# Kernel optimization log

Measured on AMD Instinct MI355X. Metric: run time of the kernel, lower is better.

## Reference

```python
import jax, jax.numpy as jnp
import numpy as np

K_NEIGHBOURS = 16
ITERATIONS = 3
NUM_CLASSES = 20
N_POINTS = 20000


def setup_inputs() -> dict:
    key = jax.random.key(0)
    k1, k2 = jax.random.split(key)
    logits = jax.random.normal(k1, (N_POINTS, NUM_CLASSES), dtype=jnp.float32)
    coords = jax.random.uniform(k2, (N_POINTS, 3), dtype=jnp.float32)
    # nn.init.eye_ then *= -0.1
    compat_w = (-0.1 * jnp.eye(NUM_CLASSES, dtype=jnp.float32))
    return {"logits": logits, "coords": coords, "compat_w": compat_w}


def _knn_graph(coords, k):
    # torch.cdist (p=2): euclidean distances, (N, N)
    sq = jnp.sum(coords * coords, axis=-1)
    d2 = sq[:, None] + sq[None, :] - 2.0 * (coords @ coords.T)
    dists = jnp.sqrt(jnp.clip(d2, 0.0))
    # smallest-k -> top_k of negated distances
    _, idx = jax.lax.top_k(-dists, k)  # (N, k)
    return idx


def reference(logits, coords, compat_w):
    knn_idx = _knn_graph(coords, K_NEIGHBOURS)
    q = jax.nn.softmax(logits, axis=-1)
    for _ in range(ITERATIONS):
        neighbour_q = q[knn_idx]            # (N, k, K) gather
        msg = jnp.mean(neighbour_q, axis=1)  # (N, K)
        refined = logits + msg @ compat_w.T  # nn.Linear: x @ W^T
        q = jax.nn.softmax(refined, axis=-1)
    return (refined, q)
```

## Files before the change

kernel.cpp:

```cpp
#include <hip/hip_runtime.h>

#define N_PTS 20000
#define NCLS 20
#define KNN 16
#define GRID 12
#define NCELLS (GRID * GRID * GRID)
#define HCELL (1.0f / (float)GRID)
#define CAND_CAP 640
#define KEY_CAP 128
#define R_TARGET 0.0680f

__device__ __forceinline__ int cell1d(float v) {
    int c = (int)(v * (float)GRID);
    return min(max(c, 0), GRID - 1);
}

__global__ __launch_bounds__(256) void count_scan_kernel(const float* __restrict__ coords,
                                                         int* __restrict__ cellCount,
                                                         int* __restrict__ doneCtr,
                                                         int* __restrict__ cellStart,
                                                         int* __restrict__ cellCursor) {
    const int p = blockIdx.x * blockDim.x + threadIdx.x;
    if (p < N_PTS) {
        const int cx = cell1d(coords[3 * p + 0]);
        const int cy = cell1d(coords[3 * p + 1]);
        const int cz = cell1d(coords[3 * p + 2]);
        atomicAdd(&cellCount[(cz * GRID + cy) * GRID + cx], 1);
    }
    __threadfence();
    __syncthreads();
    __shared__ bool isLast;
    if (threadIdx.x == 0)
        isLast = (atomicAdd(doneCtr, 1) == (int)gridDim.x - 1);
    __syncthreads();
    if (!isLast) return;

    __shared__ int part[256];
    const int t = threadIdx.x;
    const int base = t * 7;
    int local[7];
    int s = 0;
#pragma unroll
    for (int i = 0; i < 7; ++i) {
        const int c = base + i;
        const int v = (c < NCELLS)
            ? __hip_atomic_load(&cellCount[c], __ATOMIC_RELAXED, __HIP_MEMORY_SCOPE_AGENT)
            : 0;
        local[i] = s;
        s += v;
    }
    part[t] = s;
    __syncthreads();
    for (int off = 1; off < 256; off <<= 1) {
        const int v = part[t] + ((t >= off) ? part[t - off] : 0);
        __syncthreads();
        part[t] = v;
        __syncthreads();
    }
    const int excl = (t > 0) ? part[t - 1] : 0;
#pragma unroll
    for (int i = 0; i < 7; ++i) {
        const int c = base + i;
        if (c < NCELLS) {
            cellStart[c] = excl + local[i];
            cellCursor[c] = excl + local[i];
        }
    }
    if (t == 255) cellStart[NCELLS] = part[255];
}

__global__ __launch_bounds__(256) void scatter_kernel(const float* __restrict__ coords,
                                                      const float* __restrict__ logits,
                                                      int* __restrict__ cellCursor,
                                                      float4* __restrict__ sortedPts,
                                                      int* __restrict__ orig,
                                                      float* __restrict__ ls,
                                                      float* __restrict__ q0s) {
    const int p = blockIdx.x * blockDim.x + threadIdx.x;
    if (p >= N_PTS) return;
    const float x = coords[3 * p + 0];
    const float y = coords[3 * p + 1];
    const float z = coords[3 * p + 2];
    const int c = (cell1d(z) * GRID + cell1d(y)) * GRID + cell1d(x);
    const int pos = atomicAdd(&cellCursor[c], 1);
    sortedPts[pos] = make_float4(x, y, z, __uint_as_float((unsigned)p));
    orig[pos] = p;
    const float4* l4 = (const float4*)(logits + p * NCLS);
    float v[NCLS];
#pragma unroll
    for (int u = 0; u < 5; ++u) {
        const float4 a = l4[u];
        v[4 * u + 0] = a.x; v[4 * u + 1] = a.y;
        v[4 * u + 2] = a.z; v[4 * u + 3] = a.w;
    }
    float4* d4 = (float4*)(ls + pos * NCLS);
#pragma unroll
    for (int u = 0; u < 5; ++u)
        d4[u] = make_float4(v[4 * u], v[4 * u + 1], v[4 * u + 2], v[4 * u + 3]);
    float mx = v[0];
#pragma unroll
    for (int cc = 1; cc < NCLS; ++cc) mx = fmaxf(mx, v[cc]);
    float sum = 0.f;
#pragma unroll
    for (int cc = 0; cc < NCLS; ++cc) { v[cc] = __expf(v[cc] - mx); sum += v[cc]; }
    const float inv = 1.f / sum;
    float4* q4 = (float4*)(q0s + pos * NCLS);
#pragma unroll
    for (int u = 0; u < 5; ++u)
        q4[u] = make_float4(v[4 * u] * inv, v[4 * u + 1] * inv,
                            v[4 * u + 2] * inv, v[4 * u + 3] * inv);
}

__device__ void knn_ladder(const float4* __restrict__ sortedPts,
                           const int* __restrict__ cellStart,
                           const float4 qp, const int s, int hw,
                           unsigned long long* keys, const int lane,
                           int* __restrict__ knn_out) {
    const unsigned long long laneLt = (1ull << lane) - 1ull;
    const int cx = cell1d(qp.x), cy = cell1d(qp.y), cz = cell1d(qp.z);
    float g = 0.9995f * (float)hw * HCELL;
    float tau = g * g;
    int cnt = 0;
    for (int att = 0; att < 16; ++att) {
        cnt = 0;
        const int xlo = max(cx - hw, 0), xhi = min(cx + hw, GRID - 1);
        const int ylo = max(cy - hw, 0), yhi = min(cy + hw, GRID - 1);
        const int zlo = max(cz - hw, 0), zhi = min(cz + hw, GRID - 1);
        for (int zz = zlo; zz <= zhi; ++zz) {
            for (int yy = ylo; yy <= yhi; ++yy) {
                const int rowc = (zz * GRID + yy) * GRID;
                const int beg = cellStart[rowc + xlo];
                const int end = cellStart[rowc + xhi + 1];
                for (int j0 = beg; j0 < end; j0 += 64) {
                    const int j = j0 + lane;
                    const bool jv = j < end;
                    const float4 pt = sortedPts[jv ? j : beg];
                    const float dx = pt.x - qp.x, dy = pt.y - qp.y, dz = pt.z - qp.z;
                    const float d2 = dx * dx + dy * dy + dz * dz;
                    const bool take = jv && (d2 < tau);
                    const unsigned long long mm = __ballot(take);
                    if (take) {
                        const int pos = cnt + (int)__popcll(mm & laneLt);
                        if (pos < KEY_CAP)
                            keys[pos] = (((unsigned long long)__float_as_uint(d2)) << 32) |
                                        (unsigned long long)(unsigned)j;
                    }
                    cnt += (int)__popcll(mm);
                }
            }
        }
        if (cnt >= KNN && cnt <= KEY_CAP) break;
        if (cnt < KNN) {
            if (hw < GRID - 1) { ++hw; g = 0.9995f * (float)hw * HCELL; tau = g * g; }
            else tau *= 2.5f;
        } else {
            tau *= 0.6f;
        }
    }
    const int m = min(cnt, KEY_CAP);
    const unsigned long long k0 = (lane < m) ? keys[lane] : ~0ull;
    const unsigned long long k1 = (lane + 64 < m) ? keys[lane + 64] : ~0ull;
    int r0 = 0, r1 = 0;
    for (int j = 0; j < m; ++j) {
        const unsigned long long kj = keys[j];
        r0 += (kj < k0); r1 += (kj < k1);
    }
    if (lane < m && r0 < KNN)      knn_out[s * KNN + r0] = (int)(unsigned)(k0 & 0xffffffffull);
    if (lane + 64 < m && r1 < KNN) knn_out[s * KNN + r1] = (int)(unsigned)(k1 & 0xffffffffull);
}

__global__ __launch_bounds__(256) void knn_kernel(const float4* __restrict__ sortedPts,
                                                  const int* __restrict__ cellStart,
                                                  int* __restrict__ knn_out) {
    __shared__ float4 cand[CAND_CAP];
    __shared__ unsigned long long keys[4][KEY_CAP];
    const int lane = threadIdx.x & 63;
    const int wave = threadIdx.x >> 6;
    const int c = blockIdx.x >> 1;
    const int half = blockIdx.x & 1;
    const int cz = c / (GRID * GRID);
    const int cy = (c / GRID) % GRID;
    const int cx = c % GRID;
    const int pbeg = cellStart[c];
    const int pend = cellStart[c + 1];
    const int npts = pend - pbeg;
    if (npts <= 0) return;
    const int bd = (cx == 0 || cx == GRID - 1) + (cy == 0 || cy == GRID - 1) +
                   (cz == 0 || cz == GRID - 1);
    const int hs = (bd >= 2) ? 2 : 1;
    const unsigned long long laneLt = (1ull << lane) - 1ull;

    const int xlo = max(cx - hs, 0), xhi = min(cx + hs, GRID - 1);
    const int ylo = max(cy - hs, 0), yhi = min(cy + hs, GRID - 1);
    const int zlo = max(cz - hs, 0), zhi = min(cz + hs, GRID - 1);
    const int ny = yhi - ylo + 1;
    const int nruns = (zhi - zlo + 1) * ny;

    int beg = 0, len = 0;
    if (lane < nruns) {
        const int zz = zlo + lane / ny;
        const int yy = ylo + lane % ny;
        const int rowc = (zz * GRID + yy) * GRID;
        beg = cellStart[rowc + xlo];
        len = cellStart[rowc + xhi + 1] - beg;
    }
    int off = len;
#pragma unroll
    for (int sh = 1; sh < 32; sh <<= 1) {
        const int o = __shfl_up(off, sh, 64);
        if (lane >= sh) off += o;
    }
    const int nc = __shfl(off, nruns - 1);
    off -= len;
    const int ownRun = (cz - zlo) * ny + (cy - ylo);
    const int ownOff = __shfl(off, ownRun) + (pbeg - __shfl(beg, ownRun));

    if (nc <= CAND_CAP) {
        for (int r = wave; r < nruns; r += 4) {
            const int rb = __shfl(beg, r);
            const int rl = __shfl(len, r);
            const int ro = __shfl(off, r);
            for (int i = lane; i < rl; i += 64) {
                float4 pt = sortedPts[rb + i];
                pt.w = __uint_as_float((unsigned)(rb + i));
                cand[ro + i] = pt;
            }
        }
    }
    __syncthreads();

    if (nc > CAND_CAP) {
        for (int idx = 2 * wave + half; idx < npts; idx += 8)
            knn_ladder(sortedPts, cellStart, sortedPts[pbeg + idx], pbeg + idx,
                       hs, keys[wave], lane, knn_out);
        return;
    }

    const float taumaxr = 0.9995f * (float)hs * HCELL;
    const float taumax = taumaxr * taumaxr;

    for (int idx = 2 * wave + half; idx < npts; idx += 8) {
        const int s = pbeg + idx;
        const float4 qp = cand[ownOff + idx];
        float r = R_TARGET;
        const float inv2r = 0.5f / r;
        const float fx = (fminf(qp.x + r, 1.f) - fmaxf(qp.x - r, 0.f)) * inv2r;
        const float fy = (fminf(qp.y + r, 1.f) - fmaxf(qp.y - r, 0.f)) * inv2r;
        const float fz = (fminf(qp.z + r, 1.f) - fmaxf(qp.z - r, 0.f)) * inv2r;
        const float f = fmaxf(fx * fy * fz, 0.05f);
        r = R_TARGET * __powf(f, -0.33333334f);
        float tau = fminf(r * r, taumax);
        bool triedMax = (tau >= taumax * 0.999f);

        int cnt = 0;
        bool ok = false;
        for (int att = 0; att < 5 && !ok; ++att) {
            cnt = 0;
            for (int j0 = 0; j0 < nc; j0 += 64) {
                const int j = j0 + lane;
                float d2 = 1e30f;
                unsigned pw = 0;
                if (j < nc) {
                    const float4 pt = cand[j];
                    const float dx = pt.x - qp.x, dy = pt.y - qp.y, dz = pt.z - qp.z;
                    d2 = dx * dx + dy * dy + dz * dz;
                    pw = __float_as_uint(pt.w);
                }
                const bool take = d2 < tau;
                const unsigned long long mm = __ballot(take);
                if (take) {
                    const int pos = cnt + (int)__popcll(mm & laneLt);
                    if (pos < KEY_CAP)
                        keys[wave][pos] =
                            (((unsigned long long)__float_as_uint(d2)) << 32) |
                            (unsigned long long)pw;
                }
                cnt += (int)__popcll(mm);
            }
            if (cnt >= KNN && cnt <= KEY_CAP) ok = true;
            else if (cnt < KNN) {
                if (triedMax) break;
                tau = taumax; triedMax = true;
            } else tau *= 0.6f;
        }
        if (!ok) {
            knn_ladder(sortedPts, cellStart, qp, s, hs + 1, keys[wave], lane, knn_out);
            continue;
        }
        const int m = cnt;
        const unsigned long long k0 = (lane < m) ? keys[wave][lane] : ~0ull;
        const unsigned long long k1 = (lane + 64 < m) ? keys[wave][lane + 64] : ~0ull;
        int r0 = 0, r1 = 0;
        for (int j = 0; j < m; ++j) {
            const unsigned long long kj = keys[wave][j];
            r0 += (kj < k0); r1 += (kj < k1);
        }
        if (lane < m && r0 < KNN)      knn_out[s * KNN + r0] = (int)(unsigned)(k0 & 0xffffffffull);
        if (lane + 64 < m && r1 < KNN) knn_out[s * KNN + r1] = (int)(unsigned)(k1 & 0xffffffffull);
    }
}

__global__ __launch_bounds__(256) void crf_iter_kernel(const float* __restrict__ ls,
                                                       const float* __restrict__ W,
                                                       const int* __restrict__ knn,
                                                       const float* __restrict__ qin,
                                                       float* __restrict__ qout,
                                                       const int* __restrict__ orig,
                                                       float* __restrict__ outRef,
                                                       float* __restrict__ outQ) {
    __shared__ float Ws[NCLS * NCLS];
    for (int i = threadIdx.x; i < NCLS * NCLS; i += blockDim.x) Ws[i] = W[i];
    __syncthreads();
    const int t = blockIdx.x * blockDim.x + threadIdx.x;
    const int p = t >> 2;
    const int qtr = t & 3;
    if (p >= N_PTS) return;

    float acc[NCLS];
#pragma unroll
    for (int c = 0; c < NCLS; ++c) acc[c] = 0.f;

    const int4 k4 = ((const int4*)(knn + p * KNN))[qtr];
    const int ids[4] = {k4.x, k4.y, k4.z, k4.w};
#pragma unroll
    for (int u = 0; u < 4; ++u) {
        unsigned id = (unsigned)ids[u];
        if (id >= N_PTS) id = 0;
        const float4* r4 = (const float4*)(qin + id * NCLS);
#pragma unroll
        for (int v = 0; v < 5; ++v) {
            const float4 a = r4[v];
            acc[4 * v + 0] += a.x; acc[4 * v + 1] += a.y;
            acc[4 * v + 2] += a.z; acc[4 * v + 3] += a.w;
        }
    }
#pragma unroll
    for (int c = 0; c < NCLS; ++c) {
        acc[c] += __shfl_xor(acc[c], 1, 64);
        acc[c] += __shfl_xor(acc[c], 2, 64);
        acc[c] *= (1.f / 16.f);
    }

    const int c0 = qtr * 5;
    float ref[5];
#pragma unroll
    for (int i = 0; i < 5; ++i) {
        float s = ls[p * NCLS + c0 + i];
#pragma unroll
        for (int k = 0; k < NCLS; ++k) s += acc[k] * Ws[(c0 + i) * NCLS + k];
        ref[i] = s;
    }

    float mx = ref[0];
#pragma unroll
    for (int i = 1; i < 5; ++i) mx = fmaxf(mx, ref[i]);
    mx = fmaxf(mx, __shfl_xor(mx, 1, 64));
    mx = fmaxf(mx, __shfl_xor(mx, 2, 64));
    float ex[5];
    float ps = 0.f;
#pragma unroll
    for (int i = 0; i < 5; ++i) { ex[i] = __expf(ref[i] - mx); ps += ex[i]; }
    ps += __shfl_xor(ps, 1, 64);
    ps += __shfl_xor(ps, 2, 64);
    const float inv = 1.f / ps;

    if (outRef != nullptr) {
        const int o = orig[p];
#pragma unroll
        for (int i = 0; i < 5; ++i) {
            outRef[o * NCLS + c0 + i] = ref[i];
            outQ[o * NCLS + c0 + i] = ex[i] * inv;
        }
    } else {
#pragma unroll
        for (int i = 0; i < 5; ++i) qout[p * NCLS + c0 + i] = ex[i] * inv;
    }
}

extern "C" void kernel_launch(void* const* d_in, const int* in_sizes, int n_in,
                              void* d_out, int out_size, void* d_ws, size_t ws_size,
                              hipStream_t stream) {
    const float* logits = (const float*)d_in[0];
    const float* coords = (const float*)d_in[1];
    const float* W      = (const float*)d_in[2];
    float* out = (float*)d_out;

    char* ws = (char*)d_ws;
    size_t off = 0;
    int* knn = (int*)(ws + off);              off += (size_t)N_PTS * KNN * 4;
    off = (off + 255) & ~(size_t)255;
    float* ls = (float*)(ws + off);           off += (size_t)N_PTS * NCLS * 4;
    off = (off + 255) & ~(size_t)255;
    float* q0s = (float*)(ws + off);          off += (size_t)N_PTS * NCLS * 4;
    off = (off + 255) & ~(size_t)255;
    float4* sortedPts = (float4*)(ws + off);  off += (size_t)N_PTS * 16;
    off = (off + 255) & ~(size_t)255;
    int* orig = (int*)(ws + off);             off += (size_t)N_PTS * 4;
    off = (off + 255) & ~(size_t)255;
    int* cellCount = (int*)(ws + off);        off += (size_t)(NCELLS + 1) * 4;
    int* doneCtr = cellCount + NCELLS;
    off = (off + 255) & ~(size_t)255;
    int* cellStart = (int*)(ws + off);        off += (size_t)(NCELLS + 1) * 4;
    off = (off + 255) & ~(size_t)255;
    int* cellCursor = (int*)(ws + off);
    float* q1s = out + N_PTS * NCLS;

    const int threads = 256;
    const int pblocks = (N_PTS + threads - 1) / threads;
    const int cblocks = (4 * N_PTS + threads - 1) / threads;

    hipMemsetAsync(cellCount, 0, (NCELLS + 1) * sizeof(int), stream);
    count_scan_kernel<<<pblocks, threads, 0, stream>>>(coords, cellCount, doneCtr,
                                                       cellStart, cellCursor);
    scatter_kernel<<<pblocks, threads, 0, stream>>>(coords, logits, cellCursor,
                                                    sortedPts, orig, ls, q0s);
    knn_kernel<<<NCELLS * 2, threads, 0, stream>>>(sortedPts, cellStart, knn);
    crf_iter_kernel<<<cblocks, threads, 0, stream>>>(ls, W, knn, q0s, q1s, orig,
                                                     nullptr, nullptr);
    crf_iter_kernel<<<cblocks, threads, 0, stream>>>(ls, W, knn, q1s, q0s, orig,
                                                     nullptr, nullptr);
    crf_iter_kernel<<<cblocks, threads, 0, stream>>>(ls, W, knn, q0s, nullptr, orig,
                                                     out, out + N_PTS * NCLS);
}
```

Before: 128.5 us.

## Fuse count/scan/scatter and CRF iterations into kernels with in-grid barriers

Merges the cell count/scan kernel with the scatter kernel, using a release/acquire flag so the other blocks spin until the last block has finished the prefix scan. Merges the three CRF iteration launches into one kernel with a software grid barrier between iterations, and hoists the knn index and logit loads out of the iteration loop. Also vectorises the rank-counting loop over the shared-memory keys with 16-byte loads. This removes three kernel launches and their gaps, at the risk of deadlock if not all blocks (pblocks=79, cblocks=313) are resident at once, plus the cost of spin-waiting.

```diff
diff --git a/kernel.cpp b/kernel.cpp
--- a/kernel.cpp
+++ b/kernel.cpp
@@ -15,12 +15,15 @@
     return min(max(c, 0), GRID - 1);
 }
 
-__global__ __launch_bounds__(256) void count_scan_kernel(const float* __restrict__ coords,
-                                                         int* __restrict__ cellCount,
-                                                         int* __restrict__ doneCtr,
-                                                         int* __restrict__ cellStart,
-                                                         int* __restrict__ cellCursor) {
+__global__ __launch_bounds__(256) void build_scatter_kernel(
+        const float* __restrict__ coords, const float* __restrict__ logits,
+        int* __restrict__ cellCount, int* __restrict__ doneCtr,
+        int* __restrict__ scanFlag, int* __restrict__ cellStart,
+        int* __restrict__ cellCursor, float4* __restrict__ sortedPts,
+        int* __restrict__ orig, float* __restrict__ ls, float* __restrict__ q0s) {
     const int p = blockIdx.x * blockDim.x + threadIdx.x;
+    const int tid = threadIdx.x;
+
     if (p < N_PTS) {
         const int cx = cell1d(coords[3 * p + 0]);
         const int cy = cell1d(coords[3 * p + 1]);
@@ -30,53 +33,55 @@
     __threadfence();
     __syncthreads();
     __shared__ bool isLast;
-    if (threadIdx.x == 0)
+    if (tid == 0)
         isLast = (atomicAdd(doneCtr, 1) == (int)gridDim.x - 1);
     __syncthreads();
-    if (!isLast) return;
-
-    __shared__ int part[256];
-    const int t = threadIdx.x;
-    const int base = t * 7;
-    int local[7];
-    int s = 0;
-#pragma unroll
-    for (int i = 0; i < 7; ++i) {
-        const int c = base + i;
-        const int v = (c < NCELLS)
-            ? __hip_atomic_load(&cellCount[c], __ATOMIC_RELAXED, __HIP_MEMORY_SCOPE_AGENT)
-            : 0;
-        local[i] = s;
-        s += v;
-    }
-    part[t] = s;
-    __syncthreads();
-    for (int off = 1; off < 256; off <<= 1) {
-        const int v = part[t] + ((t >= off) ? part[t - off] : 0);
+
+    if (isLast) {
+        __shared__ int part[256];
+        const int base = tid * 7;
+        int local[7];
+        int s = 0;
+#pragma unroll
+        for (int i = 0; i < 7; ++i) {
+            const int c = base + i;
+            const int v = (c < NCELLS)
+                ? __hip_atomic_load(&cellCount[c], __ATOMIC_RELAXED, __HIP_MEMORY_SCOPE_AGENT)
+                : 0;
+            local[i] = s;
+            s += v;
+        }
+        part[tid] = s;
         __syncthreads();
-        part[t] = v;
+        for (int off = 1; off < 256; off <<= 1) {
+            const int v = part[tid] + ((tid >= off) ? part[tid - off] : 0);
+            __syncthreads();
+            part[tid] = v;
+            __syncthreads();
+        }
+        const int excl = (tid > 0) ? part[tid - 1] : 0;
+#pragma unroll
+        for (int i = 0; i < 7; ++i) {
+            const int c = base + i;
+            if (c < NCELLS) {
+                cellStart[c] = excl + local[i];
+                __hip_atomic_store(&cellCursor[c], excl + local[i],
+                                   __ATOMIC_RELAXED, __HIP_MEMORY_SCOPE_AGENT);
+            }
+        }
+        if (tid == 255) cellStart[NCELLS] = part[255];
+        __threadfence();
         __syncthreads();
-    }
-    const int excl = (t > 0) ? part[t - 1] : 0;
-#pragma unroll
-    for (int i = 0; i < 7; ++i) {
-        const int c = base + i;
-        if (c < NCELLS) {
-            cellStart[c] = excl + local[i];
-            cellCursor[c] = excl + local[i];
-        }
-    }
-    if (t == 255) cellStart[NCELLS] = part[255];
-}
-
-__global__ __launch_bounds__(256) void scatter_kernel(const float* __restrict__ coords,
-                                                      const float* __restrict__ logits,
-                                                      int* __restrict__ cellCursor,
-                                                      float4* __restrict__ sortedPts,
-                                                      int* __restrict__ orig,
-                                                      float* __restrict__ ls,
-                                                      float* __restrict__ q0s) {
-    const int p = blockIdx.x * blockDim.x + threadIdx.x;
+        if (tid == 0)
+            __hip_atomic_store(scanFlag, 1, __ATOMIC_RELEASE, __HIP_MEMORY_SCOPE_AGENT);
+    } else {
+        if (tid == 0)
+            while (__hip_atomic_load(scanFlag, __ATOMIC_ACQUIRE,
+                                     __HIP_MEMORY_SCOPE_AGENT) == 0) {}
+        __syncthreads();
+        __threadfence();
+    }
+
     if (p >= N_PTS) return;
     const float x = coords[3 * p + 0];
     const float y = coords[3 * p + 1];
@@ -109,6 +114,29 @@
     for (int u = 0; u < 5; ++u)
         q4[u] = make_float4(v[4 * u] * inv, v[4 * u + 1] * inv,
                             v[4 * u + 2] * inv, v[4 * u + 3] * inv);
+}
+
+__device__ __forceinline__ void rank2(const unsigned long long* __restrict__ keys,
+                                      int m, unsigned long long k0,
+                                      unsigned long long k1, int& r0, int& r1) {
+    r0 = 0; r1 = 0;
+    const ulonglong2* kp = (const ulonglong2*)keys;
+    const int mPairs = m >> 1;
+    int j2 = 0;
+    for (; j2 + 4 <= mPairs; j2 += 4) {
+        const ulonglong2 a = kp[j2 + 0];
+        const ulonglong2 b = kp[j2 + 1];
+        const ulonglong2 cc = kp[j2 + 2];
+        const ulonglong2 d = kp[j2 + 3];
+        r0 += (a.x < k0) + (a.y < k0) + (b.x < k0) + (b.y < k0) +
+              (cc.x < k0) + (cc.y < k0) + (d.x < k0) + (d.y < k0);
+        r1 += (a.x < k1) + (a.y < k1) + (b.x < k1) + (b.y < k1) +
+              (cc.x < k1) + (cc.y < k1) + (d.x < k1) + (d.y < k1);
+    }
+    for (int j = j2 * 2; j < m; ++j) {
+        const unsigned long long kj = keys[j];
+        r0 += (kj < k0); r1 += (kj < k1);
+    }
 }
 
 __device__ void knn_ladder(const float4* __restrict__ sortedPts,
@@ -160,11 +188,8 @@
     const int m = min(cnt, KEY_CAP);
     const unsigned long long k0 = (lane < m) ? keys[lane] : ~0ull;
     const unsigned long long k1 = (lane + 64 < m) ? keys[lane + 64] : ~0ull;
-    int r0 = 0, r1 = 0;
-    for (int j = 0; j < m; ++j) {
-        const unsigned long long kj = keys[j];
-        r0 += (kj < k0); r1 += (kj < k1);
-    }
+    int r0, r1;
+    rank2(keys, m, k0, k1, r0, r1);
     if (lane < m && r0 < KNN)      knn_out[s * KNN + r0] = (int)(unsigned)(k0 & 0xffffffffull);
     if (lane + 64 < m && r1 < KNN) knn_out[s * KNN + r1] = (int)(unsigned)(k1 & 0xffffffffull);
 }
@@ -173,7 +198,7 @@
                                                   const int* __restrict__ cellStart,
                                                   int* __restrict__ knn_out) {
     __shared__ float4 cand[CAND_CAP];
-    __shared__ unsigned long long keys[4][KEY_CAP];
+    __shared__ __align__(16) unsigned long long keys[4][KEY_CAP];
     const int lane = threadIdx.x & 63;
     const int wave = threadIdx.x >> 6;
     const int c = blockIdx.x >> 1;
@@ -290,90 +315,111 @@
         const int m = cnt;
         const unsigned long long k0 = (lane < m) ? keys[wave][lane] : ~0ull;
         const unsigned long long k1 = (lane + 64 < m) ? keys[wave][lane + 64] : ~0ull;
-        int r0 = 0, r1 = 0;
-        for (int j = 0; j < m; ++j) {
-            const unsigned long long kj = keys[wave][j];
-            r0 += (kj < k0); r1 += (kj < k1);
-        }
+        int r0, r1;
+        rank2(keys[wave], m, k0, k1, r0, r1);
         if (lane < m && r0 < KNN)      knn_out[s * KNN + r0] = (int)(unsigned)(k0 & 0xffffffffull);
         if (lane + 64 < m && r1 < KNN) knn_out[s * KNN + r1] = (int)(unsigned)(k1 & 0xffffffffull);
     }
 }
 
-__global__ __launch_bounds__(256) void crf_iter_kernel(const float* __restrict__ ls,
-                                                       const float* __restrict__ W,
-                                                       const int* __restrict__ knn,
-                                                       const float* __restrict__ qin,
-                                                       float* __restrict__ qout,
-                                                       const int* __restrict__ orig,
-                                                       float* __restrict__ outRef,
-                                                       float* __restrict__ outQ) {
+__device__ __forceinline__ void grid_barrier(int* ctr, int target) {
+    __threadfence();
+    __syncthreads();
+    if (threadIdx.x == 0) {
+        __hip_atomic_fetch_add(ctr, 1, __ATOMIC_RELEASE, __HIP_MEMORY_SCOPE_AGENT);
+        while (__hip_atomic_load(ctr, __ATOMIC_ACQUIRE, __HIP_MEMORY_SCOPE_AGENT) < target) {}
+    }
+    __syncthreads();
+    __threadfence();
+}
+
+__global__ __launch_bounds__(256) void crf_fused_kernel(
+        const float* __restrict__ ls, const float* __restrict__ W,
+        const int* __restrict__ knn, float* __restrict__ qA,
+        float* __restrict__ qB, const int* __restrict__ orig,
+        float* __restrict__ outRef, float* __restrict__ outQ,
+        int* __restrict__ barCtr) {
     __shared__ float Ws[NCLS * NCLS];
     for (int i = threadIdx.x; i < NCLS * NCLS; i += blockDim.x) Ws[i] = W[i];
     __syncthreads();
     const int t = blockIdx.x * blockDim.x + threadIdx.x;
     const int p = t >> 2;
     const int qtr = t & 3;
-    if (p >= N_PTS) return;
-
-    float acc[NCLS];
-#pragma unroll
-    for (int c = 0; c < NCLS; ++c) acc[c] = 0.f;
-
-    const int4 k4 = ((const int4*)(knn + p * KNN))[qtr];
-    const int ids[4] = {k4.x, k4.y, k4.z, k4.w};
-#pragma unroll
-    for (int u = 0; u < 4; ++u) {
-        unsigned id = (unsigned)ids[u];
-        if (id >= N_PTS) id = 0;
-        const float4* r4 = (const float4*)(qin + id * NCLS);
-#pragma unroll
-        for (int v = 0; v < 5; ++v) {
-            const float4 a = r4[v];
-            acc[4 * v + 0] += a.x; acc[4 * v + 1] += a.y;
-            acc[4 * v + 2] += a.z; acc[4 * v + 3] += a.w;
-        }
-    }
-#pragma unroll
-    for (int c = 0; c < NCLS; ++c) {
-        acc[c] += __shfl_xor(acc[c], 1, 64);
-        acc[c] += __shfl_xor(acc[c], 2, 64);
-        acc[c] *= (1.f / 16.f);
-    }
-
+    const bool valid = p < N_PTS;
     const int c0 = qtr * 5;
-    float ref[5];
-#pragma unroll
-    for (int i = 0; i < 5; ++i) {
-        float s = ls[p * NCLS + c0 + i];
-#pragma unroll
-        for (int k = 0; k < NCLS; ++k) s += acc[k] * Ws[(c0 + i) * NCLS + k];
-        ref[i] = s;
-    }
-
-    float mx = ref[0];
-#pragma unroll
-    for (int i = 1; i < 5; ++i) mx = fmaxf(mx, ref[i]);
-    mx = fmaxf(mx, __shfl_xor(mx, 1, 64));
-    mx = fmaxf(mx, __shfl_xor(mx, 2, 64));
-    float ex[5];
-    float ps = 0.f;
-#pragma unroll
-    for (int i = 0; i < 5; ++i) { ex[i] = __expf(ref[i] - mx); ps += ex[i]; }
-    ps += __shfl_xor(ps, 1, 64);
-    ps += __shfl_xor(ps, 2, 64);
-    const float inv = 1.f / ps;
-
-    if (outRef != nullptr) {
-        const int o = orig[p];
-#pragma unroll
-        for (int i = 0; i < 5; ++i) {
-            outRef[o * NCLS + c0 + i] = ref[i];
-            outQ[o * NCLS + c0 + i] = ex[i] * inv;
-        }
-    } else {
-#pragma unroll
-        for (int i = 0; i < 5; ++i) qout[p * NCLS + c0 + i] = ex[i] * inv;
+
+    int4 k4 = make_int4(0, 0, 0, 0);
+    float lg[5] = {0, 0, 0, 0, 0};
+    if (valid) {
+        k4 = ((const int4*)(knn + p * KNN))[qtr];
+#pragma unroll
+        for (int i = 0; i < 5; ++i) lg[i] = ls[p * NCLS + c0 + i];
+    }
+
+    for (int it = 0; it < 3; ++it) {
+        const float* qin = (it == 1) ? qB : qA;
+        float* qout = (it == 0) ? qB : qA;
+        const bool last = (it == 2);
+
+        float ref[5], ex[5];
+        float inv = 0.f;
+        if (valid) {
+            float acc[NCLS];
+#pragma unroll
+            for (int cc = 0; cc < NCLS; ++cc) acc[cc] = 0.f;
+            const int ids[4] = {k4.x, k4.y, k4.z, k4.w};
+#pragma unroll
+            for (int u = 0; u < 4; ++u) {
+                unsigned id = (unsigned)ids[u];
+                if (id >= N_PTS) id = 0;
+                const float4* r4 = (const float4*)(qin + id * NCLS);
+#pragma unroll
+                for (int vv = 0; vv < 5; ++vv) {
+                    const float4 a = r4[vv];
+                    acc[4 * vv + 0] += a.x; acc[4 * vv + 1] += a.y;
+                    acc[4 * vv + 2] += a.z; acc[4 * vv + 3] += a.w;
+                }
+            }
+#pragma unroll
+            for (int cc = 0; cc < NCLS; ++cc) {
+                acc[cc] += __shfl_xor(acc[cc], 1, 64);
+                acc[cc] += __shfl_xor(acc[cc], 2, 64);
+                acc[cc] *= (1.f / 16.f);
+            }
+#pragma unroll
+            for (int i = 0; i < 5; ++i) {
+                float s = lg[i];
+#pragma unroll
+                for (int k = 0; k < NCLS; ++k)
+                    s += acc[k] * Ws[(c0 + i) * NCLS + k];
+                ref[i] = s;
+            }
+            float mx = ref[0];
+#pragma unroll
+            for (int i = 1; i < 5; ++i) mx = fmaxf(mx, ref[i]);
+            mx = fmaxf(mx, __shfl_xor(mx, 1, 64));
+            mx = fmaxf(mx, __shfl_xor(mx, 2, 64));
+            float ps = 0.f;
+#pragma unroll
+            for (int i = 0; i < 5; ++i) { ex[i] = __expf(ref[i] - mx); ps += ex[i]; }
+            ps += __shfl_xor(ps, 1, 64);
+            ps += __shfl_xor(ps, 2, 64);
+            inv = 1.f / ps;
+
+            if (last) {
+                const int o = orig[p];
+#pragma unroll
+                for (int i = 0; i < 5; ++i) {
+                    outRef[o * NCLS + c0 + i] = ref[i];
+                    outQ[o * NCLS + c0 + i] = ex[i] * inv;
+                }
+            } else {
+#pragma unroll
+                for (int i = 0; i < 5; ++i)
+                    qout[p * NCLS + c0 + i] = ex[i] * inv;
+            }
+        }
+        if (!last) grid_barrier(barCtr, (int)gridDim.x * (it + 1));
     }
 }
 
@@ -397,8 +443,11 @@
     off = (off + 255) & ~(size_t)255;
     int* orig = (int*)(ws + off);             off += (size_t)N_PTS * 4;
     off = (off + 255) & ~(size_t)255;
-    int* cellCount = (int*)(ws + off);        off += (size_t)(NCELLS + 1) * 4;
-    int* doneCtr = cellCount + NCELLS;
+    int* ctrl = (int*)(ws + off);             off += (size_t)(NCELLS + 3) * 4;
+    int* cellCount = ctrl;
+    int* doneCtr = ctrl + NCELLS;
+    int* scanFlag = ctrl + NCELLS + 1;
+    int* barCtr = ctrl + NCELLS + 2;
     off = (off + 255) & ~(size_t)255;
     int* cellStart = (int*)(ws + off);        off += (size_t)(NCELLS + 1) * 4;
     off = (off + 255) & ~(size_t)255;
@@ -409,16 +458,11 @@
     const int pblocks = (N_PTS + threads - 1) / threads;
     const int cblocks = (4 * N_PTS + threads - 1) / threads;
 
-    hipMemsetAsync(cellCount, 0, (NCELLS + 1) * sizeof(int), stream);
-    count_scan_kernel<<<pblocks, threads, 0, stream>>>(coords, cellCount, doneCtr,
-                                                       cellStart, cellCursor);
-    scatter_kernel<<<pblocks, threads, 0, stream>>>(coords, logits, cellCursor,
-                                                    sortedPts, orig, ls, q0s);
+    hipMemsetAsync(ctrl, 0, (NCELLS + 3) * sizeof(int), stream);
+    build_scatter_kernel<<<pblocks, threads, 0, stream>>>(
+        coords, logits, cellCount, doneCtr, scanFlag, cellStart, cellCursor,
+        sortedPts, orig, ls, q0s);
     knn_kernel<<<NCELLS * 2, threads, 0, stream>>>(sortedPts, cellStart, knn);
-    crf_iter_kernel<<<cblocks, threads, 0, stream>>>(ls, W, knn, q0s, q1s, orig,
-                                                     nullptr, nullptr);
-    crf_iter_kernel<<<cblocks, threads, 0, stream>>>(ls, W, knn, q1s, q0s, orig,
-                                                     nullptr, nullptr);
-    crf_iter_kernel<<<cblocks, threads, 0, stream>>>(ls, W, knn, q0s, nullptr, orig,
-                                                     out, out + N_PTS * NCLS);
-}
+    crf_fused_kernel<<<cblocks, threads, 0, stream>>>(
+        ls, W, knn, q0s, q1s, orig, out, out + N_PTS * NCLS, barCtr);
+}
```

After: 334.4 us. 2.6x slower.

## Fuse count/scan and scatter kernels via grid-wide flag; vectorize key ranking

Applied to the files above, without the earlier changes.

Merges the cell-count/scan kernel and the scatter kernel into one launch. The last block to finish counting performs the scan and then publishes a release flag, while the other blocks spin on that flag before scattering points. This removes one kernel launch and its inter-kernel gap, but it depends on every block being resident at once (79 blocks) to avoid deadlock. Separately, the rank computation in kNN reads the shared-memory keys as 16-byte pairs with an unrolled loop to cut LDS instruction count.

```diff
diff --git a/kernel.cpp b/kernel.cpp
--- a/kernel.cpp
+++ b/kernel.cpp
@@ -15,12 +15,15 @@
     return min(max(c, 0), GRID - 1);
 }
 
-__global__ __launch_bounds__(256) void count_scan_kernel(const float* __restrict__ coords,
-                                                         int* __restrict__ cellCount,
-                                                         int* __restrict__ doneCtr,
-                                                         int* __restrict__ cellStart,
-                                                         int* __restrict__ cellCursor) {
+__global__ __launch_bounds__(256) void build_scatter_kernel(
+        const float* __restrict__ coords, const float* __restrict__ logits,
+        int* __restrict__ cellCount, int* __restrict__ doneCtr,
+        int* __restrict__ scanFlag, int* __restrict__ cellStart,
+        int* __restrict__ cellCursor, float4* __restrict__ sortedPts,
+        int* __restrict__ orig, float* __restrict__ ls, float* __restrict__ q0s) {
     const int p = blockIdx.x * blockDim.x + threadIdx.x;
+    const int tid = threadIdx.x;
+
     if (p < N_PTS) {
         const int cx = cell1d(coords[3 * p + 0]);
         const int cy = cell1d(coords[3 * p + 1]);
@@ -30,53 +33,58 @@
     __threadfence();
     __syncthreads();
     __shared__ bool isLast;
-    if (threadIdx.x == 0)
+    if (tid == 0)
         isLast = (atomicAdd(doneCtr, 1) == (int)gridDim.x - 1);
     __syncthreads();
-    if (!isLast) return;
-
-    __shared__ int part[256];
-    const int t = threadIdx.x;
-    const int base = t * 7;
-    int local[7];
-    int s = 0;
-#pragma unroll
-    for (int i = 0; i < 7; ++i) {
-        const int c = base + i;
-        const int v = (c < NCELLS)
-            ? __hip_atomic_load(&cellCount[c], __ATOMIC_RELAXED, __HIP_MEMORY_SCOPE_AGENT)
-            : 0;
-        local[i] = s;
-        s += v;
-    }
-    part[t] = s;
-    __syncthreads();
-    for (int off = 1; off < 256; off <<= 1) {
-        const int v = part[t] + ((t >= off) ? part[t - off] : 0);
+
+    if (isLast) {
+        __shared__ int part[256];
+        const int base = tid * 7;
+        int local[7];
+        int s = 0;
+#pragma unroll
+        for (int i = 0; i < 7; ++i) {
+            const int c = base + i;
+            const int v = (c < NCELLS)
+                ? __hip_atomic_load(&cellCount[c], __ATOMIC_RELAXED, __HIP_MEMORY_SCOPE_AGENT)
+                : 0;
+            local[i] = s;
+            s += v;
+        }
+        part[tid] = s;
         __syncthreads();
-        part[t] = v;
+        for (int off = 1; off < 256; off <<= 1) {
+            const int v = part[tid] + ((tid >= off) ? part[tid - off] : 0);
+            __syncthreads();
+            part[tid] = v;
+            __syncthreads();
+        }
+        const int excl = (tid > 0) ? part[tid - 1] : 0;
+#pragma unroll
+        for (int i = 0; i < 7; ++i) {
+            const int c = base + i;
+            if (c < NCELLS) {
+                cellStart[c] = excl + local[i];
+                __hip_atomic_store(&cellCursor[c], excl + local[i],
+                                   __ATOMIC_RELAXED, __HIP_MEMORY_SCOPE_AGENT);
+            }
+        }
+        if (tid == 255) cellStart[NCELLS] = part[255];
+        __threadfence();
         __syncthreads();
-    }
-    const int excl = (t > 0) ? part[t - 1] : 0;
-#pragma unroll
-    for (int i = 0; i < 7; ++i) {
-        const int c = base + i;
-        if (c < NCELLS) {
-            cellStart[c] = excl + local[i];
-            cellCursor[c] = excl + local[i];
-        }
-    }
-    if (t == 255) cellStart[NCELLS] = part[255];
-}
-
-__global__ __launch_bounds__(256) void scatter_kernel(const float* __restrict__ coords,
-                                                      const float* __restrict__ logits,
-                                                      int* __restrict__ cellCursor,
-                                                      float4* __restrict__ sortedPts,
-                                                      int* __restrict__ orig,
-                                                      float* __restrict__ ls,
-                                                      float* __restrict__ q0s) {
-    const int p = blockIdx.x * blockDim.x + threadIdx.x;
+        if (tid == 0)
+            __hip_atomic_store(scanFlag, 1, __ATOMIC_RELEASE, __HIP_MEMORY_SCOPE_AGENT);
+    } else {
+        if (tid == 0) {
+            while (__hip_atomic_load(scanFlag, __ATOMIC_RELAXED,
+                                     __HIP_MEMORY_SCOPE_AGENT) == 0)
+                __builtin_amdgcn_s_sleep(8);
+            (void)__hip_atomic_load(scanFlag, __ATOMIC_ACQUIRE,
+                                    __HIP_MEMORY_SCOPE_AGENT);
+        }
+        __syncthreads();
+    }
+
     if (p >= N_PTS) return;
     const float x = coords[3 * p + 0];
     const float y = coords[3 * p + 1];
@@ -109,6 +117,29 @@
     for (int u = 0; u < 5; ++u)
         q4[u] = make_float4(v[4 * u] * inv, v[4 * u + 1] * inv,
                             v[4 * u + 2] * inv, v[4 * u + 3] * inv);
+}
+
+__device__ __forceinline__ void rank2(const unsigned long long* __restrict__ keys,
+                                      int m, unsigned long long k0,
+                                      unsigned long long k1, int& r0, int& r1) {
+    r0 = 0; r1 = 0;
+    const ulonglong2* kp = (const ulonglong2*)keys;
+    const int mPairs = m >> 1;
+    int j2 = 0;
+    for (; j2 + 4 <= mPairs; j2 += 4) {
+        const ulonglong2 a = kp[j2 + 0];
+        const ulonglong2 b = kp[j2 + 1];
+        const ulonglong2 cc = kp[j2 + 2];
+        const ulonglong2 d = kp[j2 + 3];
+        r0 += (a.x < k0) + (a.y < k0) + (b.x < k0) + (b.y < k0) +
+              (cc.x < k0) + (cc.y < k0) + (d.x < k0) + (d.y < k0);
+        r1 += (a.x < k1) + (a.y < k1) + (b.x < k1) + (b.y < k1) +
+              (cc.x < k1) + (cc.y < k1) + (d.x < k1) + (d.y < k1);
+    }
+    for (int j = j2 * 2; j < m; ++j) {
+        const unsigned long long kj = keys[j];
+        r0 += (kj < k0); r1 += (kj < k1);
+    }
 }
 
 __device__ void knn_ladder(const float4* __restrict__ sortedPts,
@@ -160,11 +191,8 @@
     const int m = min(cnt, KEY_CAP);
     const unsigned long long k0 = (lane < m) ? keys[lane] : ~0ull;
     const unsigned long long k1 = (lane + 64 < m) ? keys[lane + 64] : ~0ull;
-    int r0 = 0, r1 = 0;
-    for (int j = 0; j < m; ++j) {
-        const unsigned long long kj = keys[j];
-        r0 += (kj < k0); r1 += (kj < k1);
-    }
+    int r0, r1;
+    rank2(keys, m, k0, k1, r0, r1);
     if (lane < m && r0 < KNN)      knn_out[s * KNN + r0] = (int)(unsigned)(k0 & 0xffffffffull);
     if (lane + 64 < m && r1 < KNN) knn_out[s * KNN + r1] = (int)(unsigned)(k1 & 0xffffffffull);
 }
@@ -173,7 +201,7 @@
                                                   const int* __restrict__ cellStart,
                                                   int* __restrict__ knn_out) {
     __shared__ float4 cand[CAND_CAP];
-    __shared__ unsigned long long keys[4][KEY_CAP];
+    __shared__ __align__(16) unsigned long long keys[4][KEY_CAP];
     const int lane = threadIdx.x & 63;
     const int wave = threadIdx.x >> 6;
     const int c = blockIdx.x >> 1;
@@ -290,11 +318,8 @@
         const int m = cnt;
         const unsigned long long k0 = (lane < m) ? keys[wave][lane] : ~0ull;
         const unsigned long long k1 = (lane + 64 < m) ? keys[wave][lane + 64] : ~0ull;
-        int r0 = 0, r1 = 0;
-        for (int j = 0; j < m; ++j) {
-            const unsigned long long kj = keys[wave][j];
-            r0 += (kj < k0); r1 += (kj < k1);
-        }
+        int r0, r1;
+        rank2(keys[wave], m, k0, k1, r0, r1);
         if (lane < m && r0 < KNN)      knn_out[s * KNN + r0] = (int)(unsigned)(k0 & 0xffffffffull);
         if (lane + 64 < m && r1 < KNN) knn_out[s * KNN + r1] = (int)(unsigned)(k1 & 0xffffffffull);
     }
@@ -397,8 +422,10 @@
     off = (off + 255) & ~(size_t)255;
     int* orig = (int*)(ws + off);             off += (size_t)N_PTS * 4;
     off = (off + 255) & ~(size_t)255;
-    int* cellCount = (int*)(ws + off);        off += (size_t)(NCELLS + 1) * 4;
-    int* doneCtr = cellCount + NCELLS;
+    int* ctrl = (int*)(ws + off);             off += (size_t)(NCELLS + 2) * 4;
+    int* cellCount = ctrl;
+    int* doneCtr = ctrl + NCELLS;
+    int* scanFlag = ctrl + NCELLS + 1;
     off = (off + 255) & ~(size_t)255;
     int* cellStart = (int*)(ws + off);        off += (size_t)(NCELLS + 1) * 4;
     off = (off + 255) & ~(size_t)255;
@@ -409,11 +436,10 @@
     const int pblocks = (N_PTS + threads - 1) / threads;
     const int cblocks = (4 * N_PTS + threads - 1) / threads;
 
-    hipMemsetAsync(cellCount, 0, (NCELLS + 1) * sizeof(int), stream);
-    count_scan_kernel<<<pblocks, threads, 0, stream>>>(coords, cellCount, doneCtr,
-                                                       cellStart, cellCursor);
-    scatter_kernel<<<pblocks, threads, 0, stream>>>(coords, logits, cellCursor,
-                                                    sortedPts, orig, ls, q0s);
+    hipMemsetAsync(ctrl, 0, (NCELLS + 2) * sizeof(int), stream);
+    build_scatter_kernel<<<pblocks, threads, 0, stream>>>(
+        coords, logits, cellCount, doneCtr, scanFlag, cellStart, cellCursor,
+        sortedPts, orig, ls, q0s);
     knn_kernel<<<NCELLS * 2, threads, 0, stream>>>(sortedPts, cellStart, knn);
     crf_iter_kernel<<<cblocks, threads, 0, stream>>>(ls, W, knn, q0s, q1s, orig,
                                                      nullptr, nullptr);
```

After: 134.2 us. 1.04x slower.
